# Kernel optimization log

Measured on AMD Instinct MI355X. Metric: run time of the kernel, lower is better.

## Reference

```python
import jax, jax.numpy as jnp
import numpy as np

B, NW, H, K = 64, 256, 768, 4
K1, Bp, AVDL = 0.1, 1.2, 50.0
ALPHA = 1.0 / H  # 1 / interaction_rep_size
BETA = 0.1


def setup_inputs() -> dict:
    key = jax.random.key(0)
    k1, k2, k3, k4, k5, k6 = jax.random.split(key, 6)
    return {
        "q_rep": jax.random.normal(k1, (B, NW, H), dtype=jnp.float32),
        "d_rep": jax.random.normal(k2, (B, NW, H), dtype=jnp.float32),
        "qtw": jax.random.uniform(k3, (B, NW), dtype=jnp.float32),
        "q_input_ids": jax.random.randint(k4, (B, NW, K), 0, 32, dtype=jnp.int32),
        "d_input_ids": jax.random.randint(k5, (B, NW, K), 0, 32, dtype=jnp.int32),
        "d_tfs": jax.random.randint(k6, (B, NW), 0, 10, dtype=jnp.int32),
    }


def _null_mask(input_ids):
    # [B, NW, 1] float mask: 0 where the whole window is zero ids
    all_zero = jnp.all(input_ids == 0, axis=2)
    return (~all_zero).astype(jnp.float32)[:, :, None]


def reference(q_rep, d_rep, qtw, q_input_ids, d_input_ids, d_tfs):
    q = q_rep * _null_mask(q_input_ids)
    d = d_rep * _null_mask(d_input_ids)

    # term-overlap scores: [B, NW, NW]
    d_expanded_tf = jnp.einsum("bqh,bdh->bqd", q, d)

    # exact match between q windows and d windows: [B, NW, NW]
    em_f = jnp.all(q_input_ids[:, :, None, :] == d_input_ids[:, None, :, :],
                   axis=3).astype(jnp.float32)

    # blended expanded term frequency, weighted by doc term frequencies
    d_tf = d_expanded_tf * (ALPHA * BETA) + em_f * (1.0 - BETA)
    tf_mult = d_tfs.astype(jnp.float32)[:, None, :]          # [B, 1, NW]
    expanded_term_df = jnp.sum(d_tf * tf_mult, axis=2)       # [B, NW]

    # BM25-like scoring
    dl = jnp.sum(d_tfs.astype(jnp.float32), axis=1, keepdims=True)  # [B, 1]
    denom = expanded_term_df * (1.0 + K1)
    nom = expanded_term_df + K1 * (1.0 - Bp + Bp * dl / AVDL)
    dtw = denom / (nom + 1e-8)
    s = jnp.sum(qtw * dtw, axis=1)                           # [B]
    return s, d_expanded_tf
```

## Files before the change

kernel.cpp:

```cpp
#include <hip/hip_runtime.h>
#include <hip/hip_bf16.h>

#define B_   64
#define NW_  256
#define H_   768

#define ALPHA_BETA     (0.1f / 768.0f)
#define OMB_           0.9f
#define K1_            0.1f
#define BP_            1.2f
#define AVDL_          50.0f

typedef __bf16 bf16x8 __attribute__((ext_vector_type(8)));
typedef float  f32x4  __attribute__((ext_vector_type(4)));

__global__ __launch_bounds__(256, 4) void gemm_score_kernel(
    const float* __restrict__ q_rep, const float* __restrict__ d_rep,
    const int* __restrict__ q_ids, const int* __restrict__ d_ids,
    const int* __restrict__ d_tfs,
    float* __restrict__ S, float* __restrict__ ws_etdf)
{
    __shared__ __align__(16) unsigned char lds[40960];

    const int tid  = threadIdx.x;
    const int wave = tid >> 6;
    const int lane = tid & 63;
    const int b  = blockIdx.z;
    const int m0 = blockIdx.y * 64;
    const int n0 = blockIdx.x * 64;

    __bf16* As = (__bf16*)(lds + wave * 10240);
    __bf16* Bs = As + 64 * 40;

    const int rq  = lane >> 2;
    const int seg = lane & 3;

    float mA[4], mB[4];
#pragma unroll
    for (int it = 0; it < 4; ++it) {
        const int row = it * 16 + rq;
        int4 qa = *(const int4*)(q_ids + ((size_t)b * NW_ + m0 + row) * 4);
        mA[it] = (qa.x == 0 && qa.y == 0 && qa.z == 0 && qa.w == 0) ? 0.f : 1.f;
        int4 da = *(const int4*)(d_ids + ((size_t)b * NW_ + n0 + row) * 4);
        mB[it] = (da.x == 0 && da.y == 0 && da.z == 0 && da.w == 0) ? 0.f : 1.f;
    }

    const float* Abase = q_rep + ((size_t)b * NW_ + m0) * H_ + wave * 192;
    const float* Bbase = d_rep + ((size_t)b * NW_ + n0) * H_ + wave * 192;

    f32x4 acc[4][4];
#pragma unroll
    for (int i = 0; i < 4; ++i)
#pragma unroll
        for (int j = 0; j < 4; ++j)
            acc[i][j] = (f32x4){0.f, 0.f, 0.f, 0.f};

    const int fr = lane & 15;
    const int fk = (lane >> 4) * 8;

    for (int kc = 0; kc < 6; ++kc) {
        float4 ra[8], rb[8];
#pragma unroll
        for (int it = 0; it < 4; ++it) {
            const float* pa = Abase + (size_t)(it * 16 + rq) * H_ + kc * 32 + seg * 8;
            ra[it * 2]     = *(const float4*)pa;
            ra[it * 2 + 1] = *(const float4*)(pa + 4);
            const float* pb = Bbase + (size_t)(it * 16 + rq) * H_ + kc * 32 + seg * 8;
            rb[it * 2]     = *(const float4*)pb;
            rb[it * 2 + 1] = *(const float4*)(pb + 4);
        }
#pragma unroll
        for (int it = 0; it < 4; ++it) {
            const int row = it * 16 + rq;
            float4 x = ra[it * 2], y = ra[it * 2 + 1];
            float m = mA[it];
            bf16x8 va;
            va[0] = (__bf16)(x.x * m); va[1] = (__bf16)(x.y * m);
            va[2] = (__bf16)(x.z * m); va[3] = (__bf16)(x.w * m);
            va[4] = (__bf16)(y.x * m); va[5] = (__bf16)(y.y * m);
            va[6] = (__bf16)(y.z * m); va[7] = (__bf16)(y.w * m);
            *(bf16x8*)&As[row * 40 + seg * 8] = va;

            float4 u = rb[it * 2], v = rb[it * 2 + 1];
            float n = mB[it];
            bf16x8 vb;
            vb[0] = (__bf16)(u.x * n); vb[1] = (__bf16)(u.y * n);
            vb[2] = (__bf16)(u.z * n); vb[3] = (__bf16)(u.w * n);
            vb[4] = (__bf16)(v.x * n); vb[5] = (__bf16)(v.y * n);
            vb[6] = (__bf16)(v.z * n); vb[7] = (__bf16)(v.w * n);
            *(bf16x8*)&Bs[row * 40 + seg * 8] = vb;
        }
        bf16x8 af[4], bfr[4];
#pragma unroll
        for (int t = 0; t < 4; ++t) {
            af[t]  = *(bf16x8*)&As[(t * 16 + fr) * 40 + fk];
            bfr[t] = *(bf16x8*)&Bs[(t * 16 + fr) * 40 + fk];
        }
#pragma unroll
        for (int i = 0; i < 4; ++i)
#pragma unroll
            for (int j = 0; j < 4; ++j)
                acc[i][j] = __builtin_amdgcn_mfma_f32_16x16x32_bf16(
                    af[i], bfr[j], acc[i][j], 0, 0, 0);
    }

    __syncthreads();

    float* T     = (float*)lds;
    int4*  qk_s  = (int4*)(lds + 17408);
    int4*  dk_s  = (int4*)(lds + 18432);
    float* tf_s  = (float*)(lds + 19456);

    if (tid < 64)
        qk_s[tid] = *(const int4*)(q_ids + ((size_t)b * NW_ + m0 + tid) * 4);
    else if (tid < 128)
        dk_s[tid - 64] = *(const int4*)(d_ids + ((size_t)b * NW_ + n0 + tid - 64) * 4);
    else if (tid < 192)
        tf_s[tid - 128] = (float)d_tfs[(size_t)b * NW_ + n0 + tid - 128];

    const int cn  = lane & 15;
    const int rb4 = (lane >> 4) * 4;
    for (int w = 0; w < 4; ++w) {
        if (wave == w) {
#pragma unroll
            for (int i = 0; i < 4; ++i)
#pragma unroll
                for (int j = 0; j < 4; ++j)
#pragma unroll
                    for (int r = 0; r < 4; ++r) {
                        const int row = i * 16 + rb4 + r;
                        const int col = j * 16 + cn;
                        if (w == 0) T[row * 68 + col]  = acc[i][j][r];
                        else        T[row * 68 + col] += acc[i][j][r];
                    }
        }
        __syncthreads();
    }

    const int r  = tid >> 2;
    const int qq = tid & 3;
    const float* Tr = &T[r * 68 + qq * 16];
    float* Srow = S + ((size_t)b * NW_ + m0 + r) * NW_ + n0 + qq * 16;
#pragma unroll
    for (int i = 0; i < 4; ++i)
        ((float4*)Srow)[i] = ((const float4*)Tr)[i];

    int4 qk = qk_s[r];
    float ps = 0.f;
#pragma unroll
    for (int i = 0; i < 16; ++i) {
        const int c = qq * 16 + i;
        int4 dk = dk_s[c];
        float em = (dk.x == qk.x && dk.y == qk.y &&
                    dk.z == qk.z && dk.w == qk.w) ? OMB_ : 0.f;
        ps += (ALPHA_BETA * Tr[i] + em) * tf_s[c];
    }
    ps += __shfl_xor(ps, 1);
    ps += __shfl_xor(ps, 2);
    if (qq == 0)
        atomicAdd(&ws_etdf[(size_t)b * NW_ + m0 + r], ps);
}

__global__ __launch_bounds__(64) void final_kernel(
    const float* __restrict__ ws_etdf, const int* __restrict__ d_tfs,
    const float* __restrict__ qtw, float* __restrict__ out)
{
    const int b = blockIdx.x;
    const int lane = threadIdx.x;

    float4 ev = *(const float4*)(ws_etdf + (size_t)b * NW_ + lane * 4);
    int4  tf4 = *(const int4*)(d_tfs   + (size_t)b * NW_ + lane * 4);
    float4 qv = *(const float4*)(qtw    + (size_t)b * NW_ + lane * 4);

    float dl = (float)(tf4.x + tf4.y + tf4.z + tf4.w);
#pragma unroll
    for (int off = 32; off; off >>= 1) dl += __shfl_xor(dl, off);

    const float c = K1_ * (1.f - BP_ + BP_ * dl / AVDL_);
    float ew[4] = {ev.x, ev.y, ev.z, ev.w};
    float qw[4] = {qv.x, qv.y, qv.z, qv.w};
    float s = 0.f;
#pragma unroll
    for (int j = 0; j < 4; ++j)
        s += qw[j] * (ew[j] * (1.f + K1_)) / (ew[j] + c + 1e-8f);
#pragma unroll
    for (int off = 32; off; off >>= 1) s += __shfl_xor(s, off);
    if (lane == 0) out[b] = s;
}

extern "C" void kernel_launch(void* const* d_in, const int* in_sizes, int n_in,
                              void* d_out, int out_size, void* d_ws, size_t ws_size,
                              hipStream_t stream)
{
    const float* q_rep = (const float*)d_in[0];
    const float* d_rep = (const float*)d_in[1];
    const float* qtw   = (const float*)d_in[2];
    const int*   q_ids = (const int*)d_in[3];
    const int*   d_ids = (const int*)d_in[4];
    const int*   d_tfs = (const int*)d_in[5];

    float* out = (float*)d_out;
    float* S   = out + B_;
    float* ws_etdf = (float*)d_ws;

    hipMemsetAsync(ws_etdf, 0, (size_t)B_ * NW_ * sizeof(float), stream);

    dim3 ggrid(NW_ / 64, NW_ / 64, B_);
    gemm_score_kernel<<<ggrid, 256, 0, stream>>>(q_rep, d_rep, q_ids, d_ids,
                                                 d_tfs, S, ws_etdf);

    final_kernel<<<B_, 64, 0, stream>>>(ws_etdf, d_tfs, qtw, out);
}
```

Measured before the change: 171.3 us.

## Use 128x128 block tiles with double-buffered LDS and move exact-match scoring to final kernel

The GEMM kernel now uses 128x128 output tiles per block, with four waves each owning a 64x64 quadrant. The split-K across waves and its LDS reduction are removed, and a register-prefetched, double-buffered LDS pipeline over 24 K-chunks replaces them. Null masks are applied to the output instead of the inputs. The exact-match and term-frequency sum moves into the final kernel, computed once per query row. This cuts redundant global loads and the serial cross-wave reduction, but the grid drops to 256 blocks with occupancy 1, which may underfill the GPU.

```diff
diff --git a/kernel.cpp b/kernel.cpp
--- a/kernel.cpp
+++ b/kernel.cpp
@@ -5,48 +5,74 @@
 #define NW_  256
 #define H_   768
 
-#define ALPHA_BETA     (0.1f / 768.0f)
-#define OMB_           0.9f
-#define K1_            0.1f
-#define BP_            1.2f
-#define AVDL_          50.0f
-
+#define AB_    (0.1f / 768.0f)
+#define OMB_   0.9f
+#define K1_    0.1f
+#define BP_    1.2f
+#define AVDL_  50.0f
+
+typedef __bf16 bf16x4 __attribute__((ext_vector_type(4)));
 typedef __bf16 bf16x8 __attribute__((ext_vector_type(8)));
 typedef float  f32x4  __attribute__((ext_vector_type(4)));
 
-__global__ __launch_bounds__(256, 4) void gemm_score_kernel(
+__global__ __launch_bounds__(256, 1) void gemm_fused(
     const float* __restrict__ q_rep, const float* __restrict__ d_rep,
     const int* __restrict__ q_ids, const int* __restrict__ d_ids,
     const int* __restrict__ d_tfs,
-    float* __restrict__ S, float* __restrict__ ws_etdf)
+    float* __restrict__ S, float* __restrict__ ws_dot)
 {
-    __shared__ __align__(16) unsigned char lds[40960];
+    __shared__ __align__(16) __bf16 As[2][128][40];
+    __shared__ __align__(16) __bf16 Bs[2][128][40];
+    __shared__ float mq_s[128];
+    __shared__ float md_s[128];
+    __shared__ float mdtf_s[128];
 
     const int tid  = threadIdx.x;
     const int wave = tid >> 6;
     const int lane = tid & 63;
-    const int b  = blockIdx.z;
-    const int m0 = blockIdx.y * 64;
-    const int n0 = blockIdx.x * 64;
-
-    __bf16* As = (__bf16*)(lds + wave * 10240);
-    __bf16* Bs = As + 64 * 40;
-
-    const int rq  = lane >> 2;
-    const int seg = lane & 3;
-
-    float mA[4], mB[4];
-#pragma unroll
-    for (int it = 0; it < 4; ++it) {
-        const int row = it * 16 + rq;
-        int4 qa = *(const int4*)(q_ids + ((size_t)b * NW_ + m0 + row) * 4);
-        mA[it] = (qa.x == 0 && qa.y == 0 && qa.z == 0 && qa.w == 0) ? 0.f : 1.f;
-        int4 da = *(const int4*)(d_ids + ((size_t)b * NW_ + n0 + row) * 4);
-        mB[it] = (da.x == 0 && da.y == 0 && da.z == 0 && da.w == 0) ? 0.f : 1.f;
-    }
-
-    const float* Abase = q_rep + ((size_t)b * NW_ + m0) * H_ + wave * 192;
-    const float* Bbase = d_rep + ((size_t)b * NW_ + n0) * H_ + wave * 192;
+    const int bid  = blockIdx.x;
+    const int b    = bid & 63;
+    const int t    = bid >> 6;
+    const int m0   = (t & 1) * 128;
+    const int n0   = (t >> 1) * 128;
+
+    if (tid < 128) {
+        int4 qa = *(const int4*)(q_ids + ((size_t)b * NW_ + m0 + tid) * 4);
+        mq_s[tid] = (qa.x == 0 && qa.y == 0 && qa.z == 0 && qa.w == 0) ? 0.f : 1.f;
+    } else {
+        const int r = tid - 128;
+        int4 da = *(const int4*)(d_ids + ((size_t)b * NW_ + n0 + r) * 4);
+        float md = (da.x == 0 && da.y == 0 && da.z == 0 && da.w == 0) ? 0.f : 1.f;
+        md_s[r]   = md;
+        mdtf_s[r] = md * (float)d_tfs[(size_t)b * NW_ + n0 + r];
+    }
+
+    const int srow = tid >> 3;
+    const int sseg = tid & 7;
+    const float* Abase = q_rep + ((size_t)b * NW_ + m0) * H_;
+    const float* Bbase = d_rep + ((size_t)b * NW_ + n0) * H_;
+
+    float4 ra[4], rb[4];
+    auto loadg = [&](int kc) {
+#pragma unroll
+        for (int i = 0; i < 4; ++i) {
+            const int row = i * 32 + srow;
+            ra[i] = *(const float4*)(Abase + (size_t)row * H_ + kc * 32 + sseg * 4);
+            rb[i] = *(const float4*)(Bbase + (size_t)row * H_ + kc * 32 + sseg * 4);
+        }
+    };
+    auto stage = [&](int buf) {
+#pragma unroll
+        for (int i = 0; i < 4; ++i) {
+            const int row = i * 32 + srow;
+            bf16x4 va = { (__bf16)ra[i].x, (__bf16)ra[i].y,
+                          (__bf16)ra[i].z, (__bf16)ra[i].w };
+            *(bf16x4*)&As[buf][row][sseg * 4] = va;
+            bf16x4 vb = { (__bf16)rb[i].x, (__bf16)rb[i].y,
+                          (__bf16)rb[i].z, (__bf16)rb[i].w };
+            *(bf16x4*)&Bs[buf][row][sseg * 4] = vb;
+        }
+    };
 
     f32x4 acc[4][4];
 #pragma unroll
@@ -57,44 +83,21 @@
 
     const int fr = lane & 15;
     const int fk = (lane >> 4) * 8;
-
-    for (int kc = 0; kc < 6; ++kc) {
-        float4 ra[8], rb[8];
-#pragma unroll
-        for (int it = 0; it < 4; ++it) {
-            const float* pa = Abase + (size_t)(it * 16 + rq) * H_ + kc * 32 + seg * 8;
-            ra[it * 2]     = *(const float4*)pa;
-            ra[it * 2 + 1] = *(const float4*)(pa + 4);
-            const float* pb = Bbase + (size_t)(it * 16 + rq) * H_ + kc * 32 + seg * 8;
-            rb[it * 2]     = *(const float4*)pb;
-            rb[it * 2 + 1] = *(const float4*)(pb + 4);
-        }
-#pragma unroll
-        for (int it = 0; it < 4; ++it) {
-            const int row = it * 16 + rq;
-            float4 x = ra[it * 2], y = ra[it * 2 + 1];
-            float m = mA[it];
-            bf16x8 va;
-            va[0] = (__bf16)(x.x * m); va[1] = (__bf16)(x.y * m);
-            va[2] = (__bf16)(x.z * m); va[3] = (__bf16)(x.w * m);
-            va[4] = (__bf16)(y.x * m); va[5] = (__bf16)(y.y * m);
-            va[6] = (__bf16)(y.z * m); va[7] = (__bf16)(y.w * m);
-            *(bf16x8*)&As[row * 40 + seg * 8] = va;
-
-            float4 u = rb[it * 2], v = rb[it * 2 + 1];
-            float n = mB[it];
-            bf16x8 vb;
-            vb[0] = (__bf16)(u.x * n); vb[1] = (__bf16)(u.y * n);
-            vb[2] = (__bf16)(u.z * n); vb[3] = (__bf16)(u.w * n);
-            vb[4] = (__bf16)(v.x * n); vb[5] = (__bf16)(v.y * n);
-            vb[6] = (__bf16)(v.z * n); vb[7] = (__bf16)(v.w * n);
-            *(bf16x8*)&Bs[row * 40 + seg * 8] = vb;
-        }
+    const int qm = wave >> 1;
+    const int qn = wave & 1;
+
+    loadg(0);
+    stage(0);
+    __syncthreads();
+
+    for (int kc = 0; kc < 24; ++kc) {
+        const int buf = kc & 1;
+        if (kc < 23) loadg(kc + 1);
         bf16x8 af[4], bfr[4];
 #pragma unroll
-        for (int t = 0; t < 4; ++t) {
-            af[t]  = *(bf16x8*)&As[(t * 16 + fr) * 40 + fk];
-            bfr[t] = *(bf16x8*)&Bs[(t * 16 + fr) * 40 + fk];
+        for (int t4 = 0; t4 < 4; ++t4) {
+            af[t4]  = *(bf16x8*)&As[buf][qm * 64 + t4 * 16 + fr][fk];
+            bfr[t4] = *(bf16x8*)&Bs[buf][qn * 64 + t4 * 16 + fr][fk];
         }
 #pragma unroll
         for (int i = 0; i < 4; ++i)
@@ -102,90 +105,89 @@
             for (int j = 0; j < 4; ++j)
                 acc[i][j] = __builtin_amdgcn_mfma_f32_16x16x32_bf16(
                     af[i], bfr[j], acc[i][j], 0, 0, 0);
-    }
-
-    __syncthreads();
-
-    float* T     = (float*)lds;
-    int4*  qk_s  = (int4*)(lds + 17408);
-    int4*  dk_s  = (int4*)(lds + 18432);
-    float* tf_s  = (float*)(lds + 19456);
-
-    if (tid < 64)
-        qk_s[tid] = *(const int4*)(q_ids + ((size_t)b * NW_ + m0 + tid) * 4);
-    else if (tid < 128)
-        dk_s[tid - 64] = *(const int4*)(d_ids + ((size_t)b * NW_ + n0 + tid - 64) * 4);
-    else if (tid < 192)
-        tf_s[tid - 128] = (float)d_tfs[(size_t)b * NW_ + n0 + tid - 128];
-
-    const int cn  = lane & 15;
-    const int rb4 = (lane >> 4) * 4;
-    for (int w = 0; w < 4; ++w) {
-        if (wave == w) {
-#pragma unroll
-            for (int i = 0; i < 4; ++i)
-#pragma unroll
-                for (int j = 0; j < 4; ++j)
-#pragma unroll
-                    for (int r = 0; r < 4; ++r) {
-                        const int row = i * 16 + rb4 + r;
-                        const int col = j * 16 + cn;
-                        if (w == 0) T[row * 68 + col]  = acc[i][j][r];
-                        else        T[row * 68 + col] += acc[i][j][r];
-                    }
-        }
+        if (kc < 23) stage(buf ^ 1);
         __syncthreads();
     }
 
-    const int r  = tid >> 2;
-    const int qq = tid & 3;
-    const float* Tr = &T[r * 68 + qq * 16];
-    float* Srow = S + ((size_t)b * NW_ + m0 + r) * NW_ + n0 + qq * 16;
+    const int cn = lane & 15;
+    const int qg = lane >> 4;
+    float md_l[4], mdtf_l[4];
+#pragma unroll
+    for (int j = 0; j < 4; ++j) {
+        const int c = qn * 64 + j * 16 + cn;
+        md_l[j]   = md_s[c];
+        mdtf_l[j] = mdtf_s[c];
+    }
+    float* Sbase = S + ((size_t)b * NW_ + m0 + qm * 64) * NW_ + n0 + qn * 64;
+
+    float rs[16];
 #pragma unroll
     for (int i = 0; i < 4; ++i)
-        ((float4*)Srow)[i] = ((const float4*)Tr)[i];
-
-    int4 qk = qk_s[r];
-    float ps = 0.f;
-#pragma unroll
-    for (int i = 0; i < 16; ++i) {
-        const int c = qq * 16 + i;
-        int4 dk = dk_s[c];
-        float em = (dk.x == qk.x && dk.y == qk.y &&
-                    dk.z == qk.z && dk.w == qk.w) ? OMB_ : 0.f;
-        ps += (ALPHA_BETA * Tr[i] + em) * tf_s[c];
-    }
-    ps += __shfl_xor(ps, 1);
-    ps += __shfl_xor(ps, 2);
-    if (qq == 0)
-        atomicAdd(&ws_etdf[(size_t)b * NW_ + m0 + r], ps);
+#pragma unroll
+        for (int r = 0; r < 4; ++r) {
+            const int row = i * 16 + qg * 4 + r;
+            const float mq = mq_s[qm * 64 + row];
+            float s = 0.f;
+#pragma unroll
+            for (int j = 0; j < 4; ++j) {
+                const float v = acc[i][j][r];
+                Sbase[(size_t)row * NW_ + j * 16 + cn] = v * mq * md_l[j];
+                s += v * mdtf_l[j];
+            }
+            rs[i * 4 + r] = s;
+        }
+#pragma unroll
+    for (int off = 1; off <= 8; off <<= 1)
+#pragma unroll
+        for (int e = 0; e < 16; ++e)
+            rs[e] += __shfl_xor(rs[e], off);
+    if (cn == 0) {
+#pragma unroll
+        for (int i = 0; i < 4; ++i)
+#pragma unroll
+            for (int r = 0; r < 4; ++r)
+                atomicAdd(&ws_dot[(size_t)b * NW_ + m0 + qm * 64 + i * 16 + qg * 4 + r],
+                          rs[i * 4 + r]);
+    }
 }
 
-__global__ __launch_bounds__(64) void final_kernel(
-    const float* __restrict__ ws_etdf, const int* __restrict__ d_tfs,
+__global__ __launch_bounds__(256) void final_kernel(
+    const float* __restrict__ ws_dot, const int* __restrict__ q_ids,
+    const int* __restrict__ d_ids, const int* __restrict__ d_tfs,
     const float* __restrict__ qtw, float* __restrict__ out)
 {
+    __shared__ int4  dk_s[256];
+    __shared__ float tf_s[256];
+    __shared__ float red[4];
+
     const int b = blockIdx.x;
-    const int lane = threadIdx.x;
-
-    float4 ev = *(const float4*)(ws_etdf + (size_t)b * NW_ + lane * 4);
-    int4  tf4 = *(const int4*)(d_tfs   + (size_t)b * NW_ + lane * 4);
-    float4 qv = *(const float4*)(qtw    + (size_t)b * NW_ + lane * 4);
-
-    float dl = (float)(tf4.x + tf4.y + tf4.z + tf4.w);
-#pragma unroll
-    for (int off = 32; off; off >>= 1) dl += __shfl_xor(dl, off);
-
+    const int t = threadIdx.x;
+    const int wave = t >> 6;
+    const int lane = t & 63;
+
+    dk_s[t] = *(const int4*)(d_ids + ((size_t)b * NW_ + t) * 4);
+    tf_s[t] = (float)d_tfs[(size_t)b * NW_ + t];
+    __syncthreads();
+
+    const int4 qk = *(const int4*)(q_ids + ((size_t)b * NW_ + t) * 4);
+    float em = 0.f, dl = 0.f;
+    for (int d = 0; d < 256; ++d) {
+        const int4 dk = dk_s[d];
+        const float tf = tf_s[d];
+        dl += tf;
+        if (dk.x == qk.x && dk.y == qk.y && dk.z == qk.z && dk.w == qk.w)
+            em += tf;
+    }
+    const float mq = (qk.x | qk.y | qk.z | qk.w) ? 1.f : 0.f;
+    const float etdf = AB_ * mq * ws_dot[(size_t)b * NW_ + t] + OMB_ * em;
     const float c = K1_ * (1.f - BP_ + BP_ * dl / AVDL_);
-    float ew[4] = {ev.x, ev.y, ev.z, ev.w};
-    float qw[4] = {qv.x, qv.y, qv.z, qv.w};
-    float s = 0.f;
-#pragma unroll
-    for (int j = 0; j < 4; ++j)
-        s += qw[j] * (ew[j] * (1.f + K1_)) / (ew[j] + c + 1e-8f);
-#pragma unroll
-    for (int off = 32; off; off >>= 1) s += __shfl_xor(s, off);
-    if (lane == 0) out[b] = s;
+    float val = qtw[(size_t)b * NW_ + t] * (etdf * (1.f + K1_)) / (etdf + c + 1e-8f);
+
+#pragma unroll
+    for (int off = 32; off; off >>= 1) val += __shfl_xor(val, off);
+    if (lane == 0) red[wave] = val;
+    __syncthreads();
+    if (t == 0) out[b] = red[0] + red[1] + red[2] + red[3];
 }
 
 extern "C" void kernel_launch(void* const* d_in, const int* in_sizes, int n_in,
@@ -201,13 +203,11 @@
 
     float* out = (float*)d_out;
     float* S   = out + B_;
-    float* ws_etdf = (float*)d_ws;
-
-    hipMemsetAsync(ws_etdf, 0, (size_t)B_ * NW_ * sizeof(float), stream);
-
-    dim3 ggrid(NW_ / 64, NW_ / 64, B_);
-    gemm_score_kernel<<<ggrid, 256, 0, stream>>>(q_rep, d_rep, q_ids, d_ids,
-                                                 d_tfs, S, ws_etdf);
-
-    final_kernel<<<B_, 64, 0, stream>>>(ws_etdf, d_tfs, qtw, out);
+    float* ws_dot = (float*)d_ws;
+
+    hipMemsetAsync(ws_dot, 0, (size_t)B_ * NW_ * sizeof(float), stream);
+
+    gemm_fused<<<256, 256, 0, stream>>>(q_rep, d_rep, q_ids, d_ids, d_tfs,
+                                        S, ws_dot);
+    final_kernel<<<B_, 256, 0, stream>>>(ws_dot, q_ids, d_ids, d_tfs, qtw, out);
 }
```

New measurement: 176.4 us. 1.03x slower.
